# Optimization experiments

Hardware: AMD Instinct MI355X
Metric: run time of the kernel (lower is better)

Reference implementation:

```python
import jax, jax.numpy as jnp
import numpy as np

GRID = 128          # voxel grid extent per axis
KERNELS = [2, 4, 8] # kernel_size == stride pooling scales
B = 4               # number of batches (point clouds)


def _pool_unpool(feats, seg, num_seg):
    # avg-pool over segment then broadcast back to original points
    sums = jax.ops.segment_sum(feats, seg, num_segments=num_seg)
    cnts = jax.ops.segment_sum(jnp.ones((feats.shape[0], 1), feats.dtype), seg, num_segments=num_seg)
    means = sums / jnp.maximum(cnts, 1.0)
    return means[seg]


def setup_inputs() -> dict:
    key = jax.random.key(0)
    k1, k2, k3, k4, k5 = jax.random.split(key, 5)
    N, C, OUT = 1_048_576, 64, 96
    mult = len(KERNELS) + 1
    feats = jax.random.normal(k1, (N, C), jnp.float32)
    coords = jax.random.randint(k2, (N, 3), 0, GRID, jnp.int32)
    batch_idx = jax.random.randint(k3, (N,), 0, B, jnp.int32)
    W = jax.random.normal(k4, (OUT, C * mult), jnp.float32) / np.sqrt(C * mult)
    b = jax.random.normal(k5, (OUT,), jnp.float32) * 0.01
    return {"feats": feats, "coords": coords, "batch_idx": batch_idx, "W": W, "b": b}


def reference(feats, coords, batch_idx, W, b):
    bidx = batch_idx.astype(jnp.int32)
    # i == 0: global average pooling per batch + MinkowskiBroadcast back to points
    cat = [_pool_unpool(feats, bidx, B)]
    # pyramid levels: AvgPool(k, stride=k) then PoolingTranspose(k, stride=k)
    for k in KERNELS:
        s = GRID // k  # pooled grid size per axis
        pc = coords // k
        seg = ((bidx * s + pc[:, 0]) * s + pc[:, 1]) * s + pc[:, 2]
        cat.append(_pool_unpool(feats, seg, B * s * s * s))
    out = jnp.concatenate(cat, axis=1)  # [N, C * (len(KERNELS)+1)]
    return out @ W.T + b                # MinkowskiLinear
```

## Files before the change

kernel.cpp:

```cpp
#include <hip/hip_runtime.h>
#include <stdint.h>


#define N_PTS   1048576
#define NB      4
#define N2SEG   (NB*64*64*64)
#define N4SEG   (NB*32*32*32)
#define N8SEG   (NB*16*16*16)

typedef unsigned int uint;

#define OFF_SUMS2  ((size_t)0)
#define OFF_CNT2   ((size_t)134217728)
#define OFF_SUMS0F ((size_t)138412032)
#define ZERO_BEG   OFF_CNT2
#define ZERO_END   ((size_t)138413056)
#define OFF_SUMS4  ((size_t)138413056)
#define OFF_MEAN4  ((size_t)155190272)
#define OFF_CNT4   ((size_t)171967488)
#define OFF_SUMS8  ((size_t)172491776)
#define OFF_MEAN8  ((size_t)174588928)
#define OFF_CNT8   ((size_t)176686080)
#define OFF_MEAN0  ((size_t)176751616)
#define OFF_WF     ((size_t)176752640)
#define WS_NEEDED  ((size_t)176801792)

#define D_S2 0u
#define D_C2 ((uint)(OFF_CNT2 / 4))
#define D_M4 ((uint)(OFF_MEAN4 / 4))
#define D_M8 ((uint)(OFF_MEAN8 / 4))
#define D_M0 ((uint)(OFF_MEAN0 / 4))

typedef short s8v __attribute__((ext_vector_type(8)));
typedef float f4v __attribute__((ext_vector_type(4)));
typedef uint  u4v __attribute__((ext_vector_type(4)));
typedef float f2v __attribute__((ext_vector_type(2)));

__device__ __forceinline__ uint pack_bf16x2(float a, float b) {
  uint ua = __float_as_uint(a), ub = __float_as_uint(b);
  ua = (ua + 0x7fffu + ((ua >> 16) & 1u)) >> 16;
  ub = (ub + 0x7fffu + ((ub >> 16) & 1u)) >> 16;
  return (ub << 16) | ua;
}
__device__ __forceinline__ float bflo(uint u) { return __uint_as_float(u << 16); }
__device__ __forceinline__ float bfhi(uint u) { return __uint_as_float(u & 0xffff0000u); }

__device__ __forceinline__ uint scale_pk(uint u, float rc) {
  return pack_bf16x2(bflo(u) * rc, bfhi(u) * rc);
}

#define ZCNT_U4 ((ZERO_END - ZERO_BEG) / 16)
__global__ __launch_bounds__(256) void k_zero_cnt(u4v* __restrict__ p) {
  u4v z = (u4v)0u;
  size_t stride = (size_t)gridDim.x * 256;
  for (size_t i = blockIdx.x * 256ull + threadIdx.x; i < ZCNT_U4; i += stride)
    __builtin_nontemporal_store(z, &p[i]);
}

__global__ __launch_bounds__(256) void k_cnt(
    const int* __restrict__ coords, const int* __restrict__ batch,
    uint* __restrict__ cnt2)
{
  int p = blockIdx.x * 256 + threadIdx.x;
  int b = batch[p];
  int x = coords[3 * p], y = coords[3 * p + 1], z = coords[3 * p + 2];
  int s2 = ((b * 64 + (x >> 1)) * 64 + (y >> 1)) * 64 + (z >> 1);
  atomicAdd(&cnt2[s2], 1u);
}

__global__ __launch_bounds__(256) void k_zmulti(
    const uint* __restrict__ cnt2, u4v* __restrict__ sums2q)
{
  int tid = blockIdx.x * 256 + threadIdx.x;
  int seg = tid >> 3, part = tid & 7;
  if (cnt2[seg] >= 2u) sums2q[seg * 8 + part] = (u4v)0u;
}

__global__ __launch_bounds__(256) void k_wf(const float* __restrict__ W,
                                            uint* __restrict__ Wf) {
  int idx = blockIdx.x * 256 + threadIdx.x;
  int d = idx & 3, l = (idx >> 2) & 63, ktnt = idx >> 8;
  int kt = ktnt / 6, nt = ktnt - kt * 6;
  int n = nt * 16 + (l & 15);
  int k = kt * 32 + (l >> 4) * 8 + d * 2;
  Wf[idx] = pack_bf16x2(W[n * 256 + k], W[n * 256 + k + 1]);
}

__global__ __launch_bounds__(256) void k_scatter2(
    const float* __restrict__ feats, const int* __restrict__ coords,
    const int* __restrict__ batch, uint* __restrict__ sums2,
    const uint* __restrict__ cnt2)
{
  int l = threadIdx.x & 63;
  int c2 = l & 31, half = l >> 5;
  int wid = (blockIdx.x * 256 + threadIdx.x) >> 6;
  int nw = (gridDim.x * 256) >> 6;
  for (int p0 = wid * 2; p0 < N_PTS; p0 += nw * 2) {
    int p = p0 + half;
    f2v f = __builtin_nontemporal_load(((const f2v*)feats) + (size_t)p * 32 + c2);
    int b = batch[p];
    int x = coords[3 * p], y = coords[3 * p + 1], z = coords[3 * p + 2];
    int s2 = ((b * 64 + (x >> 1)) * 64 + (y >> 1)) * 64 + (z >> 1);
    uint pk = pack_bf16x2(f.x, f.y);
    uint cv = cnt2[s2];
    uint* dst = sums2 + (size_t)s2 * 32 + c2;
    if (cv == 1u) {
      *dst = pk;
    } else {
      uint64_t addr = (uint64_t)(uintptr_t)dst;
      asm volatile("global_atomic_pk_add_bf16 %0, %1, off"
                   :: "v"(addr), "v"(pk));
    }
  }
}

__global__ __launch_bounds__(256) void k_down_bf(
    const uint* __restrict__ sumsF, const uint* __restrict__ cntF,
    uint* __restrict__ sumsC, uint* __restrict__ meanC,
    uint* __restrict__ cntC, int lgC, int nC)
{
  int tid = blockIdx.x * 256 + threadIdx.x;
  int sc = tid >> 5, c2 = tid & 31;
  if (sc >= nC) return;
  int CG = 1 << lgC, FG = CG << 1;
  int b = sc >> (3 * lgC);
  int r = sc & ((1 << (3 * lgC)) - 1);
  int x = r >> (2 * lgC), y = (r >> lgC) & (CG - 1), z = r & (CG - 1);
  float sx = 0.f, sy = 0.f;
  uint cn = 0;
  #pragma unroll
  for (int dx = 0; dx < 2; ++dx)
    #pragma unroll
    for (int dy = 0; dy < 2; ++dy)
      #pragma unroll
      for (int dz = 0; dz < 2; ++dz) {
        int sf = ((b * FG + 2 * x + dx) * FG + (2 * y + dy)) * FG + (2 * z + dz);
        uint cf = cntF[sf];
        if (cf) {
          uint u = sumsF[(size_t)sf * 32 + c2];
          sx += bflo(u); sy += bfhi(u);
        }
        cn += cf;
      }
  sumsC[(size_t)sc * 32 + c2] = pack_bf16x2(sx, sy);
  float rc = 1.0f / (float)(cn > 1u ? cn : 1u);
  meanC[(size_t)sc * 32 + c2] = pack_bf16x2(sx * rc, sy * rc);
  if (c2 == 0) cntC[sc] = cn;
}

__global__ __launch_bounds__(256) void k_gpart(
    const uint* __restrict__ sums8, float* __restrict__ sums0f)
{
  __shared__ float2 red[8][32];
  int b = blockIdx.x >> 5, chunk = blockIdx.x & 31;
  int t = threadIdx.x, c2 = t & 31, g = t >> 5;
  float sx = 0.f, sy = 0.f;
  for (int i = g; i < 128; i += 8) {
    uint u = sums8[(size_t)(b * 4096 + chunk * 128 + i) * 32 + c2];
    sx += bflo(u); sy += bfhi(u);
  }
  red[g][c2] = make_float2(sx, sy);
  __syncthreads();
  if (g == 0) {
    float ax = 0.f, ay = 0.f;
    #pragma unroll
    for (int i = 0; i < 8; ++i) { ax += red[i][c2].x; ay += red[i][c2].y; }
    unsafeAtomicAdd(&sums0f[b * 64 + 2 * c2], ax);
    unsafeAtomicAdd(&sums0f[b * 64 + 2 * c2 + 1], ay);
  }
}

__global__ __launch_bounds__(256) void k_fin0(
    const float* __restrict__ sums0f, const uint* __restrict__ cnt8,
    uint* __restrict__ mean0)
{
  __shared__ uint redc[256];
  __shared__ float rcs[NB];
  int t = threadIdx.x;
  uint cn = 0;
  for (int i = 0; i < 64; ++i) cn += cnt8[t * 64 + i];
  redc[t] = cn;
  __syncthreads();
  if (t < NB) {
    uint s = 0;
    for (int i = 0; i < 64; ++i) s += redc[t * 64 + i];
    rcs[t] = 1.0f / (float)(s > 1u ? s : 1u);
  }
  __syncthreads();
  if (t < 128) {
    int b = t >> 5, c2 = t & 31;
    float rc = rcs[b];
    mean0[b * 32 + c2] =
        pack_bf16x2(sums0f[b * 64 + 2 * c2] * rc, sums0f[b * 64 + 2 * c2 + 1] * rc);
  }
}

#define GPB 8

#define ISSUE(G, AF, CV) {                                                   \
    uint2 iv = idx_lds[(G) * 64 + w16pl];                                    \
    const uint4* a2 = (const uint4*)(wsb + D_S2 + iv.x * 32u);               \
    const uint4* a4 = (const uint4*)(wsb + D_M4 + (iv.y & 0x1FFFFu) * 32u);  \
    const uint4* a8 = (const uint4*)(wsb + D_M8 + (iv.y >> 17) * 32u);       \
    const uint4* a0 = (const uint4*)(wsb + D_M0 + (iv.y >> 29) * 32u);       \
    AF[0] = a0[q];  AF[1] = a0[4 + q];                                       \
    AF[2] = a2[q];  AF[3] = a2[4 + q];                                       \
    AF[4] = a4[q];  AF[5] = a4[4 + q];                                       \
    AF[6] = a8[q];  AF[7] = a8[4 + q];                                       \
    CV = wsb[D_C2 + iv.x];                                                   \
  }

#define CONSUME(G, AF, CV) {                                                 \
    float rc = 1.0f / (float)(CV > 1u ? CV : 1u);                            \
    AF[2].x = scale_pk(AF[2].x, rc); AF[2].y = scale_pk(AF[2].y, rc);        \
    AF[2].z = scale_pk(AF[2].z, rc); AF[2].w = scale_pk(AF[2].w, rc);        \
    AF[3].x = scale_pk(AF[3].x, rc); AF[3].y = scale_pk(AF[3].y, rc);        \
    AF[3].z = scale_pk(AF[3].z, rc); AF[3].w = scale_pk(AF[3].w, rc);        \
    f4v acc[6];                                                              \
    _Pragma("unroll")                                                        \
    for (int nt = 0; nt < 6; ++nt) acc[nt] = (f4v)0.0f;                      \
    _Pragma("unroll")                                                        \
    for (int kt = 0; kt < 8; ++kt) {                                         \
      s8v afr = __builtin_bit_cast(s8v, AF[kt]);                             \
      _Pragma("unroll")                                                      \
      for (int nt = 0; nt < 6; ++nt) {                                       \
        s8v bf = __builtin_bit_cast(s8v, wf[(kt * 6 + nt) * 64 + l]);        \
        acc[nt] = __builtin_amdgcn_mfma_f32_16x16x32_bf16(afr, bf, acc[nt], 0, 0, 0); \
      }                                                                      \
    }                                                                        \
    float* ob = out + (size_t)(pb + (G) * 64 + w * 16 + q * 4) * 96 + pl;    \
    _Pragma("unroll")                                                        \
    for (int nt = 0; nt < 6; ++nt)                                           \
      _Pragma("unroll")                                                      \
      for (int r = 0; r < 4; ++r)                                            \
        ob[r * 96 + nt * 16] = bn[nt] + acc[nt][r];                          \
  }

__global__ __launch_bounds__(256) void k_final(
    const int* __restrict__ coords, const int* __restrict__ batch,
    const uint* __restrict__ wsb,
    const uint4* __restrict__ Wf, const float* __restrict__ bias,
    float* __restrict__ out)
{
  __shared__ uint4 wf[3072];
  __shared__ uint2 idx_lds[512];
  int t = threadIdx.x;
  #pragma unroll
  for (int i = 0; i < 12; ++i) wf[i * 256 + t] = Wf[i * 256 + t];
  int pb = blockIdx.x * (GPB * 64);
  #pragma unroll
  for (int j = 0; j < 2; ++j) {
    int pi = t + j * 256;
    int p = pb + pi;
    int b = batch[p];
    int x = coords[3 * p], y = coords[3 * p + 1], z = coords[3 * p + 2];
    uint s2 = (uint)(((b * 64 + (x >> 1)) * 64 + (y >> 1)) * 64 + (z >> 1));
    uint s4 = (uint)(((b * 32 + (x >> 2)) * 32 + (y >> 2)) * 32 + (z >> 2));
    uint s8 = (uint)(((b * 16 + (x >> 3)) * 16 + (y >> 3)) * 16 + (z >> 3));
    idx_lds[pi] = make_uint2(s2, s4 | (s8 << 17));
  }
  int l = t & 63, w = t >> 6, pl = l & 15, q = l >> 4;
  int w16pl = w * 16 + pl;
  float bn[6];
  #pragma unroll
  for (int nt = 0; nt < 6; ++nt) bn[nt] = bias[nt * 16 + pl];
  __syncthreads();

  uint4 b0[8], b1[8], b2[8];
  uint c0, c1, c2v;
  ISSUE(0, b0, c0)
  ISSUE(1, b1, c1)
  ISSUE(2, b2, c2v)  CONSUME(0, b0, c0)
  ISSUE(3, b0, c0)   CONSUME(1, b1, c1)
  ISSUE(4, b1, c1)   CONSUME(2, b2, c2v)
  ISSUE(5, b2, c2v)  CONSUME(3, b0, c0)
  ISSUE(6, b0, c0)   CONSUME(4, b1, c1)
  ISSUE(7, b1, c1)   CONSUME(5, b2, c2v)
  CONSUME(6, b0, c0)
  CONSUME(7, b1, c1)
}

extern "C" void kernel_launch(void* const* d_in, const int* in_sizes, int n_in,
                              void* d_out, int out_size, void* d_ws, size_t ws_size,
                              hipStream_t stream)
{
  const float* feats  = (const float*)d_in[0];
  const int*   coords = (const int*)d_in[1];
  const int*   batch  = (const int*)d_in[2];
  const float* W      = (const float*)d_in[3];
  const float* bias   = (const float*)d_in[4];
  float* out = (float*)d_out;
  char* ws = (char*)d_ws;
  if (ws_size < WS_NEEDED) return;

  uint*  sums2  = (uint*)(ws + OFF_SUMS2);
  uint*  cnt2   = (uint*)(ws + OFF_CNT2);
  float* sums0f = (float*)(ws + OFF_SUMS0F);
  uint*  sums4  = (uint*)(ws + OFF_SUMS4);
  uint*  mean4  = (uint*)(ws + OFF_MEAN4);
  uint*  cnt4   = (uint*)(ws + OFF_CNT4);
  uint*  sums8  = (uint*)(ws + OFF_SUMS8);
  uint*  mean8  = (uint*)(ws + OFF_MEAN8);
  uint*  cnt8   = (uint*)(ws + OFF_CNT8);
  uint*  mean0  = (uint*)(ws + OFF_MEAN0);
  uint*  Wf     = (uint*)(ws + OFF_WF);

  k_wf<<<48, 256, 0, stream>>>(W, Wf);
  k_zero_cnt<<<1024, 256, 0, stream>>>((u4v*)(ws + ZERO_BEG));
  k_cnt<<<N_PTS / 256, 256, 0, stream>>>(coords, batch, cnt2);
  k_zmulti<<<(N2SEG * 8) / 256, 256, 0, stream>>>(cnt2, (u4v*)sums2);
  k_scatter2<<<8192, 256, 0, stream>>>(feats, coords, batch, sums2, cnt2);
  k_down_bf<<<(N4SEG * 32) / 256, 256, 0, stream>>>(sums2, cnt2, sums4, mean4, cnt4, 5, N4SEG);
  k_down_bf<<<(N8SEG * 32) / 256, 256, 0, stream>>>(sums4, cnt4, sums8, mean8, cnt8, 4, N8SEG);
  k_gpart<<<128, 256, 0, stream>>>(sums8, sums0f);
  k_fin0<<<1, 256, 0, stream>>>(sums0f, cnt8, mean0);
  k_final<<<N_PTS / (GPB * 64), 256, 0, stream>>>(
      coords, batch, (const uint*)ws, (const uint4*)Wf, bias, out);
}
```

Measured before the change: 411.5 us.

## Fold global-mean branch into per-batch bias and drop its MFMA K-slice

The global average pooling term is constant per batch, so its product with the first 64 columns of W is precomputed in k_fin0 as a per-batch bias (4x96). The final kernel then gathers and multiplies only the three pyramid levels (K=192 instead of 256), loads less weight into shared memory, stores one packed index per point and recomputes the coarser segment indices from it. This removes a quarter of the MFMAs and gathers per point and shrinks LDS use. In exchange it adds a serial per-batch dot product in a single-block kernel and a bias lookup per output row.

```diff
diff --git a/kernel.cpp b/kernel.cpp
--- a/kernel.cpp
+++ b/kernel.cpp
@@ -21,15 +21,14 @@
 #define OFF_SUMS8  ((size_t)172491776)
 #define OFF_MEAN8  ((size_t)174588928)
 #define OFF_CNT8   ((size_t)176686080)
-#define OFF_MEAN0  ((size_t)176751616)
 #define OFF_WF     ((size_t)176752640)
-#define WS_NEEDED  ((size_t)176801792)
+#define OFF_BIAS0  ((size_t)176801792)
+#define WS_NEEDED  ((size_t)176803840)
 
 #define D_S2 0u
 #define D_C2 ((uint)(OFF_CNT2 / 4))
 #define D_M4 ((uint)(OFF_MEAN4 / 4))
 #define D_M8 ((uint)(OFF_MEAN8 / 4))
-#define D_M0 ((uint)(OFF_MEAN0 / 4))
 
 typedef short s8v __attribute__((ext_vector_type(8)));
 typedef float f4v __attribute__((ext_vector_type(4)));
@@ -172,10 +171,12 @@
 
 __global__ __launch_bounds__(256) void k_fin0(
     const float* __restrict__ sums0f, const uint* __restrict__ cnt8,
-    uint* __restrict__ mean0)
+    const float* __restrict__ W, const float* __restrict__ bias,
+    float* __restrict__ bias0)
 {
   __shared__ uint redc[256];
   __shared__ float rcs[NB];
+  __shared__ float m0[NB * 64];
   int t = threadIdx.x;
   uint cn = 0;
   for (int i = 0; i < 64; ++i) cn += cnt8[t * 64 + i];
@@ -187,40 +188,46 @@
     rcs[t] = 1.0f / (float)(s > 1u ? s : 1u);
   }
   __syncthreads();
-  if (t < 128) {
-    int b = t >> 5, c2 = t & 31;
-    float rc = rcs[b];
-    mean0[b * 32 + c2] =
-        pack_bf16x2(sums0f[b * 64 + 2 * c2] * rc, sums0f[b * 64 + 2 * c2 + 1] * rc);
+  if (t < NB * 64) m0[t] = sums0f[t] * rcs[t >> 6];
+  __syncthreads();
+  for (int i = t; i < NB * 96; i += 256) {
+    int b = i / 96, o = i - b * 96;
+    float s = bias[o];
+    const float* wr = W + (size_t)o * 256;
+    #pragma unroll 8
+    for (int k = 0; k < 64; ++k) s += wr[k] * m0[b * 64 + k];
+    bias0[i] = s;
   }
 }
 
 #define GPB 8
 
 #define ISSUE(G, AF, CV) {                                                   \
-    uint2 iv = idx_lds[(G) * 64 + w16pl];                                    \
-    const uint4* a2 = (const uint4*)(wsb + D_S2 + iv.x * 32u);               \
-    const uint4* a4 = (const uint4*)(wsb + D_M4 + (iv.y & 0x1FFFFu) * 32u);  \
-    const uint4* a8 = (const uint4*)(wsb + D_M8 + (iv.y >> 17) * 32u);       \
-    const uint4* a0 = (const uint4*)(wsb + D_M0 + (iv.y >> 29) * 32u);       \
-    AF[0] = a0[q];  AF[1] = a0[4 + q];                                       \
-    AF[2] = a2[q];  AF[3] = a2[4 + q];                                       \
-    AF[4] = a4[q];  AF[5] = a4[4 + q];                                       \
-    AF[6] = a8[q];  AF[7] = a8[4 + q];                                       \
-    CV = wsb[D_C2 + iv.x];                                                   \
+    uint s2i = idx_lds[(G) * 64 + w16pl];                                    \
+    uint bb = s2i >> 18, X = (s2i >> 12) & 63u, Y = (s2i >> 6) & 63u,        \
+         Z = s2i & 63u;                                                      \
+    uint s4i = ((bb * 32 + (X >> 1)) * 32 + (Y >> 1)) * 32 + (Z >> 1);       \
+    uint s8i = ((bb * 16 + (X >> 2)) * 16 + (Y >> 2)) * 16 + (Z >> 2);       \
+    const uint4* a2 = (const uint4*)(wsb + D_S2 + s2i * 32u);                \
+    const uint4* a4 = (const uint4*)(wsb + D_M4 + s4i * 32u);                \
+    const uint4* a8 = (const uint4*)(wsb + D_M8 + s8i * 32u);                \
+    AF[0] = a2[q];  AF[1] = a2[4 + q];                                       \
+    AF[2] = a4[q];  AF[3] = a4[4 + q];                                       \
+    AF[4] = a8[q];  AF[5] = a8[4 + q];                                       \
+    CV = wsb[D_C2 + s2i];                                                    \
   }
 
 #define CONSUME(G, AF, CV) {                                                 \
     float rc = 1.0f / (float)(CV > 1u ? CV : 1u);                            \
-    AF[2].x = scale_pk(AF[2].x, rc); AF[2].y = scale_pk(AF[2].y, rc);        \
-    AF[2].z = scale_pk(AF[2].z, rc); AF[2].w = scale_pk(AF[2].w, rc);        \
-    AF[3].x = scale_pk(AF[3].x, rc); AF[3].y = scale_pk(AF[3].y, rc);        \
-    AF[3].z = scale_pk(AF[3].z, rc); AF[3].w = scale_pk(AF[3].w, rc);        \
+    AF[0].x = scale_pk(AF[0].x, rc); AF[0].y = scale_pk(AF[0].y, rc);        \
+    AF[0].z = scale_pk(AF[0].z, rc); AF[0].w = scale_pk(AF[0].w, rc);        \
+    AF[1].x = scale_pk(AF[1].x, rc); AF[1].y = scale_pk(AF[1].y, rc);        \
+    AF[1].z = scale_pk(AF[1].z, rc); AF[1].w = scale_pk(AF[1].w, rc);        \
     f4v acc[6];                                                              \
     _Pragma("unroll")                                                        \
     for (int nt = 0; nt < 6; ++nt) acc[nt] = (f4v)0.0f;                      \
     _Pragma("unroll")                                                        \
-    for (int kt = 0; kt < 8; ++kt) {                                         \
+    for (int kt = 0; kt < 6; ++kt) {                                         \
       s8v afr = __builtin_bit_cast(s8v, AF[kt]);                             \
       _Pragma("unroll")                                                      \
       for (int nt = 0; nt < 6; ++nt) {                                       \
@@ -228,25 +235,35 @@
         acc[nt] = __builtin_amdgcn_mfma_f32_16x16x32_bf16(afr, bf, acc[nt], 0, 0, 0); \
       }                                                                      \
     }                                                                        \
-    float* ob = out + (size_t)(pb + (G) * 64 + w * 16 + q * 4) * 96 + pl;    \
+    int base = (G) * 64 + w * 16 + q * 4;                                    \
+    float* ob = out + (size_t)(pb + base) * 96 + pl;                         \
     _Pragma("unroll")                                                        \
-    for (int nt = 0; nt < 6; ++nt)                                           \
+    for (int r = 0; r < 4; ++r) {                                            \
+      uint br = idx_lds[base + r] >> 18;                                     \
+      const float* bp = &bias0_l[br * 96 + pl];                              \
       _Pragma("unroll")                                                      \
-      for (int r = 0; r < 4; ++r)                                            \
-        ob[r * 96 + nt * 16] = bn[nt] + acc[nt][r];                          \
+      for (int nt = 0; nt < 6; ++nt)                                         \
+        ob[r * 96 + nt * 16] = bp[nt * 16] + acc[nt][r];                     \
+    }                                                                        \
   }
 
 __global__ __launch_bounds__(256) void k_final(
     const int* __restrict__ coords, const int* __restrict__ batch,
     const uint* __restrict__ wsb,
-    const uint4* __restrict__ Wf, const float* __restrict__ bias,
+    const uint4* __restrict__ Wf, const float* __restrict__ bias0,
     float* __restrict__ out)
 {
-  __shared__ uint4 wf[3072];
-  __shared__ uint2 idx_lds[512];
+  __shared__ uint4 wf[2304];
+  __shared__ uint idx_lds[512];
+  __shared__ float bias0_l[NB * 96];
   int t = threadIdx.x;
   #pragma unroll
-  for (int i = 0; i < 12; ++i) wf[i * 256 + t] = Wf[i * 256 + t];
+  for (int i = 0; i < 9; ++i) wf[i * 256 + t] = Wf[768 + i * 256 + t];
+  #pragma unroll
+  for (int j = 0; j < 2; ++j) {
+    int i = t + j * 256;
+    if (i < NB * 96) bias0_l[i] = bias0[i];
+  }
   int pb = blockIdx.x * (GPB * 64);
   #pragma unroll
   for (int j = 0; j < 2; ++j) {
@@ -254,19 +271,13 @@
     int p = pb + pi;
     int b = batch[p];
     int x = coords[3 * p], y = coords[3 * p + 1], z = coords[3 * p + 2];
-    uint s2 = (uint)(((b * 64 + (x >> 1)) * 64 + (y >> 1)) * 64 + (z >> 1));
-    uint s4 = (uint)(((b * 32 + (x >> 2)) * 32 + (y >> 2)) * 32 + (z >> 2));
-    uint s8 = (uint)(((b * 16 + (x >> 3)) * 16 + (y >> 3)) * 16 + (z >> 3));
-    idx_lds[pi] = make_uint2(s2, s4 | (s8 << 17));
+    idx_lds[pi] = (uint)(((b * 64 + (x >> 1)) * 64 + (y >> 1)) * 64 + (z >> 1));
   }
   int l = t & 63, w = t >> 6, pl = l & 15, q = l >> 4;
   int w16pl = w * 16 + pl;
-  float bn[6];
-  #pragma unroll
-  for (int nt = 0; nt < 6; ++nt) bn[nt] = bias[nt * 16 + pl];
-  __syncthreads();
-
-  uint4 b0[8], b1[8], b2[8];
+  __syncthreads();
+
+  uint4 b0[6], b1[6], b2[6];
   uint c0, c1, c2v;
   ISSUE(0, b0, c0)
   ISSUE(1, b1, c1)
@@ -302,8 +313,8 @@
   uint*  sums8  = (uint*)(ws + OFF_SUMS8);
   uint*  mean8  = (uint*)(ws + OFF_MEAN8);
   uint*  cnt8   = (uint*)(ws + OFF_CNT8);
-  uint*  mean0  = (uint*)(ws + OFF_MEAN0);
   uint*  Wf     = (uint*)(ws + OFF_WF);
+  float* bias0  = (float*)(ws + OFF_BIAS0);
 
   k_wf<<<48, 256, 0, stream>>>(W, Wf);
   k_zero_cnt<<<1024, 256, 0, stream>>>((u4v*)(ws + ZERO_BEG));
@@ -313,7 +324,7 @@
   k_down_bf<<<(N4SEG * 32) / 256, 256, 0, stream>>>(sums2, cnt2, sums4, mean4, cnt4, 5, N4SEG);
   k_down_bf<<<(N8SEG * 32) / 256, 256, 0, stream>>>(sums4, cnt4, sums8, mean8, cnt8, 4, N8SEG);
   k_gpart<<<128, 256, 0, stream>>>(sums8, sums0f);
-  k_fin0<<<1, 256, 0, stream>>>(sums0f, cnt8, mean0);
+  k_fin0<<<1, 256, 0, stream>>>(sums0f, cnt8, W, bias, bias0);
   k_final<<<N_PTS / (GPB * 64), 256, 0, stream>>>(
-      coords, batch, (const uint*)ws, (const uint4*)Wf, bias, out);
-}
+      coords, batch, (const uint*)ws, (const uint4*)Wf, bias0, out);
+}
```

Result: faster. 396.7 us (-3.6%).
